# Performance work log

Hardware: AMD Instinct MI355X
Metric: run time of the kernel (lower is better)

Reference implementation:

```python
import jax, jax.numpy as jnp
import numpy as np

D_MODEL, N_HEADS, D_FF = 1024, 16, 4096
SCALE = 0.1          # lookup-activation input quantization step
NUM_BITS = 8
LEVELS = 1 << NUM_BITS   # 256
HALF = LEVELS // 2       # 128
MAX_EXP = 4
EPS = 1e-5


def pow2_weight(key, shape, max_exp=MAX_EXP):
    """Ternary power-of-two weights: values in {0, +/-2^{-e}}, e in [max_exp, max_exp+3].
    Exponent range keeps fan-in-1024 outputs O(1)."""
    k1, k2 = jax.random.split(key)
    sign = jax.random.randint(k1, shape, -1, 2).astype(jnp.float32)  # {-1,0,1}
    e = jax.random.randint(k2, shape, max_exp, max_exp + 4).astype(jnp.float32)
    return sign * jnp.exp2(-e)


def setup_inputs() -> dict:
    key = jax.random.key(0)
    ks = jax.random.split(key, 8)
    x = jax.random.normal(ks[0], (4, 2048, D_MODEL), dtype=jnp.float32)
    return {
        "x": x,
        "ln1_g": jnp.ones((D_MODEL,), jnp.float32),
        "ln1_b": jnp.zeros((D_MODEL,), jnp.float32),
        "wq": pow2_weight(ks[1], (D_MODEL, D_MODEL)),
        "wk": pow2_weight(ks[2], (D_MODEL, D_MODEL)),
        "wv": pow2_weight(ks[3], (D_MODEL, D_MODEL)),
        "wo": pow2_weight(ks[4], (D_MODEL, D_MODEL)),
        "ln2_g": jnp.ones((D_MODEL,), jnp.float32),
        "ln2_b": jnp.zeros((D_MODEL,), jnp.float32),
        "w1": pow2_weight(ks[5], (D_MODEL, D_FF)),
        "w2": pow2_weight(ks[6], (D_FF, D_MODEL)),
    }


def _layernorm(x, g, b):
    mu = jnp.mean(x, axis=-1, keepdims=True)
    var = jnp.var(x, axis=-1, keepdims=True)
    return (x - mu) * jax.lax.rsqrt(var + EPS) * g + b


def _lookup_act(x):
    # StructuredLookupActivation: quantize input to 2^num_bits levels, gather from
    # a precomputed GELU table (proved via Lasso lookup in the SNARK).
    grid = (jnp.arange(LEVELS, dtype=jnp.float32) - HALF) * SCALE
    table = jax.nn.gelu(grid)
    idx = jnp.clip(jnp.round(x / SCALE).astype(jnp.int32) + HALF, 0, LEVELS - 1)
    return table[idx]


def _linear_attention(x, wq, wk, wv, wo):
    B, S, D = x.shape
    H, Dh = N_HEADS, D // N_HEADS
    q = (x @ wq).reshape(B, S, H, Dh)
    k = (x @ wk).reshape(B, S, H, Dh)
    v = (x @ wv).reshape(B, S, H, Dh)
    # elu+1 feature map -> O(S*Dh^2) linear attention (no [S,S] scores)
    phi_q = jax.nn.elu(q) + 1.0
    phi_k = jax.nn.elu(k) + 1.0
    kv = jnp.einsum('bshd,bshe->bhde', phi_k, v)          # [B,H,Dh,Dh]
    z = jnp.sum(phi_k, axis=1)                            # [B,H,Dh]
    num = jnp.einsum('bshd,bhde->bshe', phi_q, kv)        # [B,S,H,Dh]
    den = jnp.einsum('bshd,bhd->bsh', phi_q, z)[..., None] + 1e-6
    out = (num / den).reshape(B, S, D)
    return out @ wo


def reference(x, ln1_g, ln1_b, wq, wk, wv, wo, ln2_g, ln2_b, w1, w2):
    # norm -> linear attention -> residual
    x = x + _linear_attention(_layernorm(x, ln1_g, ln1_b), wq, wk, wv, wo)
    # norm -> ternary FFN with lookup activation -> residual
    h = _layernorm(x, ln2_g, ln2_b)
    x = x + (_lookup_act(h @ w1) @ w2)
    return x
```

## Files before the change

kernel.cpp:

```cpp
#include <hip/hip_runtime.h>
#include <cstdint>
#include <cstddef>


#define D_MODEL 1024
#define SEQ     2048
#define BATCH   4
#define NTOK    8192
#define NHEADS  16
#define DH      64
#define DFF     4096
#define KVCH    16
#define CHROWS  (SEQ / KVCH)
#define PSTRIDE 4160

typedef _Float16 half8 __attribute__((ext_vector_type(8)));
typedef float f32x4 __attribute__((ext_vector_type(4)));
typedef unsigned int u32x4 __attribute__((ext_vector_type(4)));

__device__ __forceinline__ unsigned short f2h(float x) {
  _Float16 h = (_Float16)x;
  union { _Float16 h; unsigned short u; } c; c.h = h; return c.u;
}
__device__ __forceinline__ float h2f(unsigned short u) {
  union { unsigned short u; _Float16 h; } c; c.u = u; return (float)c.h;
}

__device__ __forceinline__ float phi_act(float x) {
  return x > 0.f ? x + 1.f : expf(x);
}

__device__ __forceinline__ float gelu_exact(float v) {
  float c = 0.7978845608028654f;
  float t = tanhf(c * (v + 0.044715f * v * v * v));
  return 0.5f * v * (1.f + t);
}

__device__ __forceinline__ void gl_lds16(const void* g, void* l) {
  __builtin_amdgcn_global_load_lds(
      (const __attribute__((address_space(1))) unsigned int*)g,
      (__attribute__((address_space(3))) unsigned int*)l, 16, 0, 0);
}

__device__ __forceinline__ void convT_body(const float* __restrict__ W,
                                           unsigned short* __restrict__ WT,
                                           int K, int N, int bx, int by, int t) {
  __shared__ float tile[64][65];
  int kb = by << 6, nb = bx << 6;
  int rr = t >> 4, cc = (t & 15) << 2;
#pragma unroll
  for (int i = 0; i < 4; ++i) {
    int r = rr + (i << 4);
    float4 v = *(const float4*)(W + (size_t)(kb + r) * N + nb + cc);
    tile[r][cc] = v.x; tile[r][cc + 1] = v.y; tile[r][cc + 2] = v.z; tile[r][cc + 3] = v.w;
  }
  __syncthreads();
#pragma unroll
  for (int i = 0; i < 4; ++i) {
    int n = rr + (i << 4);
    ushort4 o;
    o.x = f2h(tile[cc + 0][n]); o.y = f2h(tile[cc + 1][n]);
    o.z = f2h(tile[cc + 2][n]); o.w = f2h(tile[cc + 3][n]);
    *(ushort4*)(WT + (size_t)(nb + n) * K + kb + cc) = o;
  }
}

__device__ __forceinline__ void ln_body(const float* __restrict__ X,
                                        const float* __restrict__ g,
                                        const float* __restrict__ b,
                                        unsigned short* __restrict__ Y,
                                        int tok, int t) {
  const float4* xr = (const float4*)(X + (size_t)tok * D_MODEL);
  float4 v = xr[t];
  float s  = v.x + v.y + v.z + v.w;
  float s2 = v.x * v.x + v.y * v.y + v.z * v.z + v.w * v.w;
#pragma unroll
  for (int o = 32; o > 0; o >>= 1) {
    s  += __shfl_down(s, o);
    s2 += __shfl_down(s2, o);
  }
  __shared__ float red[8];
  __shared__ float mu_s, rs_s;
  int wid = t >> 6;
  if ((t & 63) == 0) { red[wid] = s; red[wid + 4] = s2; }
  __syncthreads();
  if (t == 0) {
    float ts  = red[0] + red[1] + red[2] + red[3];
    float ts2 = red[4] + red[5] + red[6] + red[7];
    float mu  = ts * (1.f / D_MODEL);
    float var = ts2 * (1.f / D_MODEL) - mu * mu;
    mu_s = mu;
    rs_s = rsqrtf(var + 1e-5f);
  }
  __syncthreads();
  float mu = mu_s, rs = rs_s;
  float4 gv = ((const float4*)g)[t];
  float4 bv = ((const float4*)b)[t];
  ushort4 hv;
  hv.x = f2h((v.x - mu) * rs * gv.x + bv.x);
  hv.y = f2h((v.y - mu) * rs * gv.y + bv.y);
  hv.z = f2h((v.z - mu) * rs * gv.z + bv.z);
  hv.w = f2h((v.w - mu) * rs * gv.w + bv.w);
  ((ushort4*)(Y + (size_t)tok * D_MODEL))[t] = hv;
}

__global__ __launch_bounds__(256) void prep_kernel(
    const float* __restrict__ wq, const float* __restrict__ wk,
    const float* __restrict__ wv, const float* __restrict__ wo,
    const float* __restrict__ w1, const float* __restrict__ w2,
    const float* __restrict__ x, const float* __restrict__ g,
    const float* __restrict__ b,
    unsigned short* __restrict__ wqkvT, unsigned short* __restrict__ woT,
    unsigned short* __restrict__ w1T, unsigned short* __restrict__ w2T,
    unsigned short* __restrict__ xn) {
  int f = blockIdx.x;
  int t = threadIdx.x;
  if (f < 1024) {
    int job = f >> 8, r = f & 255;
    const float* W = (job == 0) ? wq : (job == 1) ? wk : (job == 2) ? wv : wo;
    unsigned short* D = (job == 3) ? woT
                                   : wqkvT + (size_t)job * D_MODEL * D_MODEL;
    convT_body(W, D, D_MODEL, D_MODEL, r & 15, r >> 4, t);
  } else if (f < 2048) {
    int r = f - 1024;
    convT_body(w1, w1T, D_MODEL, DFF, r & 63, r >> 6, t);
  } else if (f < 3072) {
    int r = f - 2048;
    convT_body(w2, w2T, DFF, D_MODEL, r & 15, r >> 4, t);
  } else {
    ln_body(x, g, b, xn, f - 3072, t);
  }
}

__global__ __launch_bounds__(256) void ln_kernel(const float* __restrict__ X,
                                                 const float* __restrict__ g,
                                                 const float* __restrict__ b,
                                                 unsigned short* __restrict__ Y) {
  ln_body(X, g, b, Y, blockIdx.x, threadIdx.x);
}

template <int EP, int BK>
__global__ __launch_bounds__(256, (BK == 64) ? 4 : 2) void mfma_gemm(
    const unsigned short* __restrict__ A,
    const unsigned short* __restrict__ BT,
    void* Cv, const float* R, int N, int K) {
  constexpr int SEGS = BK / 8;
  constexpr int RPC  = 64 / SEGS;
  constexpr int NJ   = 32 / RPC;
  __shared__ unsigned short smem[2 * 128 * BK];
  __shared__ float gtab[EP == 3 ? 256 : 1];
  unsigned short* sA = smem;
  unsigned short* sB = smem + 128 * BK;

  int t = threadIdx.x;
  if (EP == 3) gtab[t & 255] = gelu_exact((float)((t & 255) - 128) * 0.1f);

  int bm, bn;
  {
    int L = blockIdx.y * gridDim.x + blockIdx.x;
    if ((gridDim.y & 7) == 0) {
      int xcd = L & 7, wi = L >> 3;
      int mPerX = gridDim.y >> 3;
      bm = xcd * mPerX + wi / gridDim.x;
      bn = wi % gridDim.x;
    } else {
      bn = blockIdx.x; bm = blockIdx.y;
    }
  }

  int w = t >> 6, l = t & 63;
  int lrow = l / SEGS;
  int lseg = l & (SEGS - 1);
  int m0 = bm << 7;
  int n0 = bn << 7;
  size_t strideB = (size_t)K * 2;

  const char* gA[NJ]; const char* gB[NJ];
  int ldsOff[NJ];
#pragma unroll
  for (int j = 0; j < NJ; ++j) {
    int row = (w << 5) + j * RPC + lrow;
    int gso = (lseg ^ (row & 7)) << 4;
    gA[j] = (const char*)A + (size_t)(m0 + row) * strideB + gso;
    gB[j] = (const char*)BT + (size_t)(n0 + row) * strideB + gso;
    ldsOff[j] = ((w << 5) + j * RPC) * BK;
  }

  int wm = w >> 1, wn = w & 1;
  int m16 = l & 15, qd = l >> 4;

  f32x4 acc[4][4];
#pragma unroll
  for (int i = 0; i < 4; ++i)
#pragma unroll
    for (int j = 0; j < 4; ++j) acc[i][j] = (f32x4){0.f, 0.f, 0.f, 0.f};

  for (int k0 = 0; k0 < K; k0 += BK) {
    size_t kb = (size_t)k0 * 2;
#pragma unroll
    for (int j = 0; j < NJ; ++j) {
      gl_lds16(gA[j] + kb, sA + ldsOff[j]);
      gl_lds16(gB[j] + kb, sB + ldsOff[j]);
    }
    __syncthreads();
#pragma unroll
    for (int kk = 0; kk < BK / 32; ++kk) {
      int ksb = (kk << 2) + qd;
      half8 af[4], bf[4];
#pragma unroll
      for (int mt = 0; mt < 4; ++mt) {
        int r = (wm << 6) + (mt << 4) + m16;
        int slot = ksb ^ (r & 7);
        af[mt] = *(const half8*)(sA + r * BK + (slot << 3));
      }
#pragma unroll
      for (int nt = 0; nt < 4; ++nt) {
        int r = (wn << 6) + (nt << 4) + m16;
        int slot = ksb ^ (r & 7);
        bf[nt] = *(const half8*)(sB + r * BK + (slot << 3));
      }
#pragma unroll
      for (int mt = 0; mt < 4; ++mt)
#pragma unroll
        for (int nt = 0; nt < 4; ++nt)
          acc[mt][nt] = __builtin_amdgcn_mfma_f32_16x16x32_f16(af[mt], bf[nt], acc[mt][nt], 0, 0, 0);
    }
    __syncthreads();
  }

  int sel = n0 >> 10;
  size_t slab = (size_t)sel * ((size_t)NTOK * D_MODEL);
  int colL = (n0 & 1023) + (wn << 6) + m16;

  int colBase = n0 + (wn << 6) + m16;
#pragma unroll
  for (int mt = 0; mt < 4; ++mt) {
    int rBase = m0 + (wm << 6) + (mt << 4) + (qd << 2);
#pragma unroll
    for (int nt = 0; nt < 4; ++nt) {
      int col = colBase + (nt << 4);
#pragma unroll
      for (int i = 0; i < 4; ++i) {
        float v = acc[mt][nt][i];
        if (EP == 4) {
          if (sel < 2) v = phi_act(v);
          size_t idx = slab + (size_t)(rBase + i) * D_MODEL + colL + (nt << 4);
          ((unsigned short*)Cv)[idx] = f2h(v);
        } else {
          size_t idx = (size_t)(rBase + i) * N + col;
          if (EP == 2)      ((float*)Cv)[idx] = R[idx] + v;
          else if (EP == 3) {
            float r = rintf(v / 0.1f);
            int iq = (int)r + 128;
            iq = iq < 0 ? 0 : (iq > 255 ? 255 : iq);
            ((unsigned short*)Cv)[idx] = f2h(gtab[iq]);
          } else          ((float*)Cv)[idx] = v;
        }
      }
    }
  }
}

__global__ __launch_bounds__(256) void kvz_partial(const unsigned short* __restrict__ PK,
                                                   const unsigned short* __restrict__ V,
                                                   float* __restrict__ P) {
  int c = blockIdx.x, bh = blockIdx.y;
  int b = bh >> 4, h = bh & 15;
  __shared__ float pk[8][64];
  __shared__ float vv[8][64];
  int t = threadIdx.x;
  const size_t base = ((size_t)b * SEQ + (size_t)c * CHROWS) * D_MODEL + h * DH;
  int u = t & 127;
  int lrow = u >> 4;
  int lcol = (u & 15) << 2;
  bool isV = (t >= 128);
  const unsigned short* src = isV ? V : PK;
  int dkb = (t >> 4) << 2;
  int deb = (t & 15) << 2;
  float acc[4][4] = {};
  float zacc = 0.f;
  for (int s0 = 0; s0 < CHROWS; s0 += 8) {
    ushort4 ld = *(const ushort4*)(src + base + (size_t)(s0 + lrow) * D_MODEL + lcol);
    float f0 = h2f(ld.x), f1 = h2f(ld.y), f2 = h2f(ld.z), f3 = h2f(ld.w);
    __syncthreads();
    if (isV) { vv[lrow][lcol] = f0; vv[lrow][lcol+1] = f1; vv[lrow][lcol+2] = f2; vv[lrow][lcol+3] = f3; }
    else     { pk[lrow][lcol] = f0; pk[lrow][lcol+1] = f1; pk[lrow][lcol+2] = f2; pk[lrow][lcol+3] = f3; }
    __syncthreads();
#pragma unroll
    for (int ss = 0; ss < 8; ++ss) {
      float4 a  = *(const float4*)&pk[ss][dkb];
      float4 bb = *(const float4*)&vv[ss][deb];
      acc[0][0] += a.x * bb.x; acc[0][1] += a.x * bb.y; acc[0][2] += a.x * bb.z; acc[0][3] += a.x * bb.w;
      acc[1][0] += a.y * bb.x; acc[1][1] += a.y * bb.y; acc[1][2] += a.y * bb.z; acc[1][3] += a.y * bb.w;
      acc[2][0] += a.z * bb.x; acc[2][1] += a.z * bb.y; acc[2][2] += a.z * bb.z; acc[2][3] += a.z * bb.w;
      acc[3][0] += a.w * bb.x; acc[3][1] += a.w * bb.y; acc[3][2] += a.w * bb.z; acc[3][3] += a.w * bb.w;
    }
    if (t < 64) {
#pragma unroll
      for (int ss = 0; ss < 8; ++ss) zacc += pk[ss][t];
    }
  }
  float* Pb = P + ((size_t)c * 64 + bh) * PSTRIDE;
#pragma unroll
  for (int i = 0; i < 4; ++i) {
    float4 o; o.x = acc[i][0]; o.y = acc[i][1]; o.z = acc[i][2]; o.w = acc[i][3];
    *(float4*)(Pb + (size_t)(dkb + i) * DH + deb) = o;
  }
  if (t < 64) Pb[4096 + t] = zacc;
}

__global__ __launch_bounds__(256) void kvz_reduce(const float* __restrict__ P,
                                                  unsigned short* __restrict__ KVT,
                                                  float* __restrict__ Z) {
  int bh = blockIdx.x;
  int t = threadIdx.x;
  for (int i = t; i < PSTRIDE; i += 256) {
    float s = 0.f;
#pragma unroll
    for (int c = 0; c < KVCH; ++c)
      s += P[((size_t)c * 64 + bh) * PSTRIDE + i];
    if (i < 4096) {
      int d = i >> 6, e = i & 63;
      KVT[(size_t)bh * 4096 + e * 64 + d] = f2h(s);
    } else {
      Z[(size_t)bh * 64 + (i - 4096)] = s;
    }
  }
}

__global__ __launch_bounds__(256) void attn_mfma(const unsigned short* __restrict__ PQ,
                                                 const unsigned short* __restrict__ KVT,
                                                 const float* __restrict__ Z,
                                                 unsigned short* __restrict__ O) {
  __shared__ unsigned short sA[256 * 64];
  __shared__ unsigned short sB[64 * 64];
  __shared__ float zsh[64];
  __shared__ float dsh[256];
  int t = threadIdx.x;
  int tok0 = blockIdx.x << 8;
  int h = blockIdx.y;
  int b = tok0 >> 11;
  int bh = b * NHEADS + h;

  const unsigned short* aSrc = PQ + (size_t)tok0 * D_MODEL + h * DH;
#pragma unroll
  for (int j = 0; j < 8; ++j) {
    int id = t + (j << 8);
    int r = id >> 3, s = id & 7;
    u32x4 v = *(const u32x4*)(aSrc + (size_t)r * D_MODEL + (s << 3));
    *(u32x4*)(sA + r * 64 + ((s ^ (r & 7)) << 3)) = v;
  }
  const unsigned short* bSrc = KVT + (size_t)bh * 4096;
#pragma unroll
  for (int j = 0; j < 2; ++j) {
    int id = t + (j << 8);
    int r = id >> 3, s = id & 7;
    u32x4 v = *(const u32x4*)(bSrc + r * 64 + (s << 3));
    *(u32x4*)(sB + r * 64 + ((s ^ (r & 7)) << 3)) = v;
  }
  if (t < 64) zsh[t] = Z[(size_t)bh * 64 + t];
  __syncthreads();

  {
    float d_ = 1e-6f;
#pragma unroll
    for (int s = 0; s < 8; ++s) {
      half8 q = *(const half8*)(sA + t * 64 + (((s ^ (t & 7))) << 3));
#pragma unroll
      for (int j = 0; j < 8; ++j)
        d_ += (float)q[j] * zsh[(s << 3) + j];
    }
    dsh[t] = d_;
  }

  int w = t >> 6, l = t & 63;
  int m16 = l & 15, qd = l >> 4;
  int wrow = w << 6;

  f32x4 acc[4][4];
#pragma unroll
  for (int i = 0; i < 4; ++i)
#pragma unroll
    for (int j = 0; j < 4; ++j) acc[i][j] = (f32x4){0.f, 0.f, 0.f, 0.f};

#pragma unroll
  for (int kk = 0; kk < 2; ++kk) {
    int ksb = (kk << 2) + qd;
    half8 af[4], bf[4];
#pragma unroll
    for (int mt = 0; mt < 4; ++mt) {
      int r = wrow + (mt << 4) + m16;
      af[mt] = *(const half8*)(sA + r * 64 + ((ksb ^ (r & 7)) << 3));
    }
#pragma unroll
    for (int nt = 0; nt < 4; ++nt) {
      int r = (nt << 4) + m16;
      bf[nt] = *(const half8*)(sB + r * 64 + ((ksb ^ (r & 7)) << 3));
    }
#pragma unroll
    for (int mt = 0; mt < 4; ++mt)
#pragma unroll
      for (int nt = 0; nt < 4; ++nt)
        acc[mt][nt] = __builtin_amdgcn_mfma_f32_16x16x32_f16(af[mt], bf[nt], acc[mt][nt], 0, 0, 0);
  }
  __syncthreads();

#pragma unroll
  for (int mt = 0; mt < 4; ++mt) {
#pragma unroll
    for (int i = 0; i < 4; ++i) {
      int rloc = wrow + (mt << 4) + (qd << 2) + i;
      float rcp = 1.f / dsh[rloc];
      size_t obase = (size_t)(tok0 + rloc) * D_MODEL + h * DH + m16;
#pragma unroll
      for (int nt = 0; nt < 4; ++nt)
        O[obase + (nt << 4)] = f2h(acc[mt][nt][i] * rcp);
    }
  }
}

extern "C" void kernel_launch(void* const* d_in, const int* in_sizes, int n_in,
                              void* d_out, int out_size, void* d_ws, size_t ws_size,
                              hipStream_t stream) {
  const float* x    = (const float*)d_in[0];
  const float* ln1g = (const float*)d_in[1];
  const float* ln1b = (const float*)d_in[2];
  const float* wq   = (const float*)d_in[3];
  const float* wk   = (const float*)d_in[4];
  const float* wv   = (const float*)d_in[5];
  const float* wo   = (const float*)d_in[6];
  const float* ln2g = (const float*)d_in[7];
  const float* ln2b = (const float*)d_in[8];
  const float* w1   = (const float*)d_in[9];
  const float* w2   = (const float*)d_in[10];
  float* out = (float*)d_out;
  char* ws = (char*)d_ws;

  const size_t MB = 1024 * 1024;
  unsigned short* xn   = (unsigned short*)(ws);
  unsigned short* qkv  = (unsigned short*)(ws + 32 * MB);
  unsigned short* phiq = qkv;
  unsigned short* phik = qkv + (size_t)NTOK * D_MODEL;
  unsigned short* vbuf = qkv + 2 * (size_t)NTOK * D_MODEL;
  unsigned short* ffn  = (unsigned short*)(ws + 32 * MB);
  unsigned short* w1T  = (unsigned short*)(ws + 96 * MB);
  unsigned short* w2T  = (unsigned short*)(ws + 104 * MB);
  unsigned short* woT  = (unsigned short*)(ws + 128 * MB);

  unsigned short* wqkvT = (unsigned short*)d_out;
  float* kvP = (float*)((char*)d_out + 6 * MB);
  unsigned short* kvT16 = (unsigned short*)((char*)d_out + 24 * MB);
  float* z   = (float*)((char*)d_out + 25 * MB);

  dim3 blk(256);

  prep_kernel<<<dim3(3072 + NTOK), blk, 0, stream>>>(
      wq, wk, wv, wo, w1, w2, x, ln1g, ln1b, wqkvT, woT, w1T, w2T, xn);

  dim3 gQKV(3 * D_MODEL / 128, NTOK / 128);
  mfma_gemm<4, 64><<<gQKV, blk, 0, stream>>>(xn, wqkvT, qkv, nullptr, 3 * D_MODEL, D_MODEL);

  kvz_partial<<<dim3(KVCH, BATCH * NHEADS), blk, 0, stream>>>(phik, vbuf, kvP);
  kvz_reduce<<<BATCH * NHEADS, blk, 0, stream>>>(kvP, kvT16, z);

  attn_mfma<<<dim3(NTOK / 256, NHEADS), blk, 0, stream>>>(phiq, kvT16, z, xn);

  dim3 gD(D_MODEL / 128, NTOK / 128);
  mfma_gemm<2, 128><<<gD, blk, 0, stream>>>(xn, woT, out, x, D_MODEL, D_MODEL);

  ln_kernel<<<NTOK, blk, 0, stream>>>(out, ln2g, ln2b, xn);

  dim3 gF(DFF / 128, NTOK / 128);
  mfma_gemm<3, 64><<<gF, blk, 0, stream>>>(xn, w1T, ffn, nullptr, DFF, D_MODEL);

  mfma_gemm<2, 128><<<gD, blk, 0, stream>>>(ffn, w2T, out, out, D_MODEL, DFF);
}
```

Measured before the change: 449.3 us.

## Split-K final FFN GEMM with atomics and fuse kv reduction via atomicAdd

The separate kvz_reduce kernel is replaced by atomicAdd accumulation of per-chunk KV and Z partials into buffers zeroed in the prep kernel. attn_mfma now reads the fp32 KV directly and transposes it into LDS while converting to fp16. The final w2 GEMM becomes a two-way split-K with BK=64, accumulating atomically into out, which already holds the residual, to raise parallelism. The cost is atomic traffic and non-deterministic float summation order.

```diff
diff --git a/kernel.cpp b/kernel.cpp
--- a/kernel.cpp
+++ b/kernel.cpp
@@ -12,7 +12,6 @@
 #define DFF     4096
 #define KVCH    16
 #define CHROWS  (SEQ / KVCH)
-#define PSTRIDE 4160
 
 typedef _Float16 half8 __attribute__((ext_vector_type(8)));
 typedef float f32x4 __attribute__((ext_vector_type(4)));
@@ -112,7 +111,7 @@
     const float* __restrict__ b,
     unsigned short* __restrict__ wqkvT, unsigned short* __restrict__ woT,
     unsigned short* __restrict__ w1T, unsigned short* __restrict__ w2T,
-    unsigned short* __restrict__ xn) {
+    unsigned short* __restrict__ xn, float* __restrict__ kvz) {
   int f = blockIdx.x;
   int t = threadIdx.x;
   if (f < 1024) {
@@ -127,8 +126,11 @@
   } else if (f < 3072) {
     int r = f - 2048;
     convT_body(w2, w2T, DFF, D_MODEL, r & 15, r >> 4, t);
+  } else if (f < 3072 + NTOK) {
+    ln_body(x, g, b, xn, f - 3072, t);
   } else {
-    ln_body(x, g, b, xn, f - 3072, t);
+    int r = f - 3072 - NTOK;
+    ((f32x4*)kvz)[(size_t)r * 256 + t] = (f32x4){0.f, 0.f, 0.f, 0.f};
   }
 }
 
@@ -143,7 +145,7 @@
 __global__ __launch_bounds__(256, (BK == 64) ? 4 : 2) void mfma_gemm(
     const unsigned short* __restrict__ A,
     const unsigned short* __restrict__ BT,
-    void* Cv, const float* R, int N, int K) {
+    void* Cv, const float* R, int N, int K, int Kst) {
   constexpr int SEGS = BK / 8;
   constexpr int RPC  = 64 / SEGS;
   constexpr int NJ   = 32 / RPC;
@@ -173,7 +175,8 @@
   int lseg = l & (SEGS - 1);
   int m0 = bm << 7;
   int n0 = bn << 7;
-  size_t strideB = (size_t)K * 2;
+  size_t strideB = (size_t)Kst * 2;
+  size_t kzOff = (size_t)blockIdx.z * K * 2;
 
   const char* gA[NJ]; const char* gB[NJ];
   int ldsOff[NJ];
@@ -181,8 +184,8 @@
   for (int j = 0; j < NJ; ++j) {
     int row = (w << 5) + j * RPC + lrow;
     int gso = (lseg ^ (row & 7)) << 4;
-    gA[j] = (const char*)A + (size_t)(m0 + row) * strideB + gso;
-    gB[j] = (const char*)BT + (size_t)(n0 + row) * strideB + gso;
+    gA[j] = (const char*)A + (size_t)(m0 + row) * strideB + kzOff + gso;
+    gB[j] = (const char*)BT + (size_t)(n0 + row) * strideB + kzOff + gso;
     ldsOff[j] = ((w << 5) + j * RPC) * BK;
   }
 
@@ -249,6 +252,7 @@
         } else {
           size_t idx = (size_t)(rBase + i) * N + col;
           if (EP == 2)      ((float*)Cv)[idx] = R[idx] + v;
+          else if (EP == 5) atomicAdd(((float*)Cv) + idx, v);
           else if (EP == 3) {
             float r = rintf(v / 0.1f);
             int iq = (int)r + 128;
@@ -263,7 +267,8 @@
 
 __global__ __launch_bounds__(256) void kvz_partial(const unsigned short* __restrict__ PK,
                                                    const unsigned short* __restrict__ V,
-                                                   float* __restrict__ P) {
+                                                   float* __restrict__ KV,
+                                                   float* __restrict__ Z) {
   int c = blockIdx.x, bh = blockIdx.y;
   int b = bh >> 4, h = bh & 15;
   __shared__ float pk[8][64];
@@ -300,36 +305,17 @@
       for (int ss = 0; ss < 8; ++ss) zacc += pk[ss][t];
     }
   }
-  float* Pb = P + ((size_t)c * 64 + bh) * PSTRIDE;
-#pragma unroll
-  for (int i = 0; i < 4; ++i) {
-    float4 o; o.x = acc[i][0]; o.y = acc[i][1]; o.z = acc[i][2]; o.w = acc[i][3];
-    *(float4*)(Pb + (size_t)(dkb + i) * DH + deb) = o;
-  }
-  if (t < 64) Pb[4096 + t] = zacc;
-}
-
-__global__ __launch_bounds__(256) void kvz_reduce(const float* __restrict__ P,
-                                                  unsigned short* __restrict__ KVT,
-                                                  float* __restrict__ Z) {
-  int bh = blockIdx.x;
-  int t = threadIdx.x;
-  for (int i = t; i < PSTRIDE; i += 256) {
-    float s = 0.f;
-#pragma unroll
-    for (int c = 0; c < KVCH; ++c)
-      s += P[((size_t)c * 64 + bh) * PSTRIDE + i];
-    if (i < 4096) {
-      int d = i >> 6, e = i & 63;
-      KVT[(size_t)bh * 4096 + e * 64 + d] = f2h(s);
-    } else {
-      Z[(size_t)bh * 64 + (i - 4096)] = s;
-    }
-  }
+  float* kvb = KV + (size_t)bh * 4096;
+#pragma unroll
+  for (int i = 0; i < 4; ++i)
+#pragma unroll
+    for (int j = 0; j < 4; ++j)
+      atomicAdd(kvb + (size_t)(dkb + i) * DH + deb + j, acc[i][j]);
+  if (t < 64) atomicAdd(Z + (size_t)bh * 64 + t, zacc);
 }
 
 __global__ __launch_bounds__(256) void attn_mfma(const unsigned short* __restrict__ PQ,
-                                                 const unsigned short* __restrict__ KVT,
+                                                 const float* __restrict__ KV,
                                                  const float* __restrict__ Z,
                                                  unsigned short* __restrict__ O) {
   __shared__ unsigned short sA[256 * 64];
@@ -350,13 +336,19 @@
     u32x4 v = *(const u32x4*)(aSrc + (size_t)r * D_MODEL + (s << 3));
     *(u32x4*)(sA + r * 64 + ((s ^ (r & 7)) << 3)) = v;
   }
-  const unsigned short* bSrc = KVT + (size_t)bh * 4096;
-#pragma unroll
-  for (int j = 0; j < 2; ++j) {
-    int id = t + (j << 8);
-    int r = id >> 3, s = id & 7;
-    u32x4 v = *(const u32x4*)(bSrc + r * 64 + (s << 3));
-    *(u32x4*)(sB + r * 64 + ((s ^ (r & 7)) << 3)) = v;
+  {
+    const float* kvb = KV + (size_t)bh * 4096;
+    int d = t & 63, eq = t >> 6;
+    int sg = d >> 3, dp = d & 7;
+#pragma unroll
+    for (int j = 0; j < 4; ++j) {
+      int e0 = (eq << 4) + (j << 2);
+      float4 v = *(const float4*)(kvb + (size_t)d * DH + e0);
+      sB[(e0 + 0) * 64 + ((sg ^ ((e0 + 0) & 7)) << 3) + dp] = f2h(v.x);
+      sB[(e0 + 1) * 64 + ((sg ^ ((e0 + 1) & 7)) << 3) + dp] = f2h(v.y);
+      sB[(e0 + 2) * 64 + ((sg ^ ((e0 + 2) & 7)) << 3) + dp] = f2h(v.z);
+      sB[(e0 + 3) * 64 + ((sg ^ ((e0 + 3) & 7)) << 3) + dp] = f2h(v.w);
+    }
   }
   if (t < 64) zsh[t] = Z[(size_t)bh * 64 + t];
   __syncthreads();
@@ -448,30 +440,33 @@
   unsigned short* woT  = (unsigned short*)(ws + 128 * MB);
 
   unsigned short* wqkvT = (unsigned short*)d_out;
-  float* kvP = (float*)((char*)d_out + 6 * MB);
-  unsigned short* kvT16 = (unsigned short*)((char*)d_out + 24 * MB);
-  float* z   = (float*)((char*)d_out + 25 * MB);
+  float* kv = (float*)((char*)d_out + 6 * MB);
+  float* z  = (float*)((char*)d_out + 7 * MB);
 
   dim3 blk(256);
 
-  prep_kernel<<<dim3(3072 + NTOK), blk, 0, stream>>>(
-      wq, wk, wv, wo, w1, w2, x, ln1g, ln1b, wqkvT, woT, w1T, w2T, xn);
+  prep_kernel<<<dim3(3072 + NTOK + 260), blk, 0, stream>>>(
+      wq, wk, wv, wo, w1, w2, x, ln1g, ln1b, wqkvT, woT, w1T, w2T, xn, kv);
 
   dim3 gQKV(3 * D_MODEL / 128, NTOK / 128);
-  mfma_gemm<4, 64><<<gQKV, blk, 0, stream>>>(xn, wqkvT, qkv, nullptr, 3 * D_MODEL, D_MODEL);
-
-  kvz_partial<<<dim3(KVCH, BATCH * NHEADS), blk, 0, stream>>>(phik, vbuf, kvP);
-  kvz_reduce<<<BATCH * NHEADS, blk, 0, stream>>>(kvP, kvT16, z);
-
-  attn_mfma<<<dim3(NTOK / 256, NHEADS), blk, 0, stream>>>(phiq, kvT16, z, xn);
+  mfma_gemm<4, 64><<<gQKV, blk, 0, stream>>>(xn, wqkvT, qkv, nullptr,
+                                             3 * D_MODEL, D_MODEL, D_MODEL);
+
+  kvz_partial<<<dim3(KVCH, BATCH * NHEADS), blk, 0, stream>>>(phik, vbuf, kv, z);
+
+  attn_mfma<<<dim3(NTOK / 256, NHEADS), blk, 0, stream>>>(phiq, kv, z, xn);
 
   dim3 gD(D_MODEL / 128, NTOK / 128);
-  mfma_gemm<2, 128><<<gD, blk, 0, stream>>>(xn, woT, out, x, D_MODEL, D_MODEL);
+  mfma_gemm<2, 128><<<gD, blk, 0, stream>>>(xn, woT, out, x,
+                                            D_MODEL, D_MODEL, D_MODEL);
 
   ln_kernel<<<NTOK, blk, 0, stream>>>(out, ln2g, ln2b, xn);
 
   dim3 gF(DFF / 128, NTOK / 128);
-  mfma_gemm<3, 64><<<gF, blk, 0, stream>>>(xn, w1T, ffn, nullptr, DFF, D_MODEL);
-
-  mfma_gemm<2, 128><<<gD, blk, 0, stream>>>(ffn, w2T, out, out, D_MODEL, DFF);
-}
+  mfma_gemm<3, 64><<<gF, blk, 0, stream>>>(xn, w1T, ffn, nullptr,
+                                           DFF, D_MODEL, D_MODEL);
+
+  dim3 gD2(D_MODEL / 128, NTOK / 128, 2);
+  mfma_gemm<5, 64><<<gD2, blk, 0, stream>>>(ffn, w2T, out, nullptr,
+                                            D_MODEL, DFF / 2, DFF);
+}
```

After: 488.3 us. 1.09x slower.
